# Kernel tuning notes

Measured on AMD Instinct MI355X. Metric: run time of the kernel, lower is better.

## Reference

```python
import jax, jax.numpy as jnp
import numpy as np

B, S = 128, 512          # batch, sequence length
VOCAB, E, H = 50000, 300, 64  # vocab, embed dim, hidden_size (num conv filters)
KMAX = H // 2 + 2 - 1    # largest kernel height = (H-1)//2 + 2 = 33


def setup_inputs() -> dict:
    key = jax.random.key(0)
    ks = jax.random.split(key, 6)
    x = jax.random.randint(ks[0], (B, 1, S), 0, VOCAB)                  # token ids, [B,1,S]
    emb = jax.random.normal(ks[1], (VOCAB, E), jnp.float32) * 0.1       # frozen embedding table
    Wconv = jax.random.normal(ks[2], (H, KMAX, E), jnp.float32) * 0.05  # padded conv kernels; conv i uses rows [:i//2+2]
    bconv = jax.random.normal(ks[3], (H,), jnp.float32) * 0.05
    Wlin = jax.random.normal(ks[4], (1, H), jnp.float32) * 0.1
    blin = jax.random.normal(ks[5], (1,), jnp.float32) * 0.1
    return {"x": x, "emb": emb, "Wconv": Wconv, "bconv": bconv, "Wlin": Wlin, "blin": blin}


def reference(x, emb, Wconv, bconv, Wlin, blin):
    # Embedding lookup: [B,1,S] -> [B,S,E] (channel dim of 1 is implicit)
    e = emb[x[:, 0]]
    feats = []
    for i in range(H):  # static loop over structurally distinct kernel sizes
        k = i // 2 + 2                      # kernel height for conv i
        w = Wconv[i, :k]                    # [k,E], valid (unpadded) kernel rows
        # Conv2d with kernel (k,E) on [B,1,S,E] == sliding dot product over positions.
        proj = jnp.einsum('bse,ke->bsk', e, w)          # [B,S,k]
        L = S - k + 1                                   # valid output length
        y = sum(proj[:, j:j + L, j] for j in range(k)) + bconv[i]  # [B,L]
        # tanh then topk(k=1, dim=1) == max over positions
        feats.append(jnp.max(jnp.tanh(y), axis=1))      # [B]
    h = jnp.stack(feats, axis=1)                        # [B,H]
    return jax.nn.sigmoid(h @ Wlin.T + blin)            # [B,1]
```

## Files before the change

### kernel.cpp

```cpp
#include <hip/hip_runtime.h>


#define SS     512
#define EE     300
#define HH     64
#define KMAXW  33
#define LP     168
#define HALFSZ 215040

typedef __attribute__((ext_vector_type(8))) short bf16x8;
typedef __attribute__((ext_vector_type(4))) float f32x4;

__device__ __forceinline__ unsigned short f2bf(float f) {
    unsigned u = __float_as_uint(f);
    unsigned r = ((u >> 16) & 1u) + 0x7FFFu;
    return (unsigned short)((u + r) >> 16);
}

__global__ __launch_bounds__(256) void prep_weights(const float* __restrict__ Wconv,
                                                    unsigned short* __restrict__ wsB) {
    int idx = blockIdx.x * 256 + threadIdx.x;
    int r    = idx & 7;
    int lane = (idx >> 3) & 63;
    int gs   = idx >> 9;
    int h    = gs / 420;
    int ww   = gs - h * 420;
    int g, t;
    if      (ww < 45)  { g = 0; t = ww;       }
    else if (ww < 130) { g = 1; t = ww - 45;  }
    else if (ww < 255) { g = 2; t = ww - 130; }
    else               { g = 3; t = ww - 255; }
    int j = t / 5, u = t - j * 5;
    int i  = g * 16 + (lane & 15);
    int ki = i / 2 + 2;
    int kk = (lane >> 4) * 8 + r;
    int e  = h * 160 + u * 32 + kk;
    float v = 0.f;
    if (e < EE && j < ki) v = Wconv[(i * KMAXW + j) * EE + e];
    wsB[idx] = f2bf(v);
}

#define MFMA(A, Bf, C) __builtin_amdgcn_mfma_f32_16x16x32_bf16((A), (Bf), (C), 0, 0, 0)

template<bool SEC>
__device__ __forceinline__ void do5(const unsigned short* lb, int j,
                                    const unsigned short* __restrict__ bp,
                                    int pbase, int sbase, f32x4 acc[3][2]) {
    #pragma unroll
    for (int u = 0; u < 5; ++u) {
        const unsigned short* lr = lb + j * LP + u * 32;
        bf16x8 a0 = *(const bf16x8*)(lr);
        bf16x8 a1 = *(const bf16x8*)(lr + 16 * LP);
        bf16x8 a2 = *(const bf16x8*)(lr + 32 * LP);
        bf16x8 bP = *(const bf16x8*)(bp + (pbase + j * 5 + u) * 512);
        acc[0][0] = MFMA(a0, bP, acc[0][0]);
        acc[1][0] = MFMA(a1, bP, acc[1][0]);
        acc[2][0] = MFMA(a2, bP, acc[2][0]);
        if (SEC) {
            bf16x8 bS = *(const bf16x8*)(bp + (sbase + j * 5 + u) * 512);
            acc[0][1] = MFMA(a0, bS, acc[0][1]);
            acc[1][1] = MFMA(a1, bS, acc[1][1]);
            acc[2][1] = MFMA(a2, bS, acc[2][1]);
        }
    }
}

__global__ __launch_bounds__(256, 3) void conv_fused(const int* __restrict__ x,
                                                     const float* __restrict__ emb,
                                                     const unsigned short* __restrict__ wsB,
                                                     const float* __restrict__ bconv,
                                                     float* __restrict__ wsF) {
    __shared__ __align__(16) unsigned short At[128 * LP];

    int b     = blockIdx.x / 6;
    int slice = blockIdx.x - b * 6;
    int t0    = slice * 96;

    int lane = threadIdx.x & 63;
    int w    = threadIdx.x >> 6;
    int p    = w >> 1;
    int h2   = w & 1;
    int m = lane & 15, q = lane >> 4;

    f32x4 acc[3][2] = {};

    const unsigned short* lb = At + (p * 48 + m) * LP + q * 8;

    for (int eh = 0; eh < 2; ++eh) {
        if (eh) __syncthreads();

        #pragma unroll
        for (int it = 0; it < 10; ++it) {
            int idx = threadIdx.x + it * 256;
            int rr = idx / 20, c = idx - rr * 20;
            int srow = t0 + rr;
            bf16x8 v = {0, 0, 0, 0, 0, 0, 0, 0};
            if (srow < SS) {
                int tok = x[b * SS + srow];
                const float* ep = emb + (long)tok * EE + eh * 160 + c * 8;
                if (eh == 0 || c < 17) {
                    float4 f0 = ((const float4*)ep)[0];
                    float4 f1 = ((const float4*)ep)[1];
                    v[0] = f2bf(f0.x); v[1] = f2bf(f0.y); v[2] = f2bf(f0.z); v[3] = f2bf(f0.w);
                    v[4] = f2bf(f1.x); v[5] = f2bf(f1.y); v[6] = f2bf(f1.z); v[7] = f2bf(f1.w);
                } else if (c == 17) {
                    float4 f0 = ((const float4*)ep)[0];
                    v[0] = f2bf(f0.x); v[1] = f2bf(f0.y); v[2] = f2bf(f0.z); v[3] = f2bf(f0.w);
                }
            }
            *(bf16x8*)&At[rr * LP + c * 8] = v;
        }
        __syncthreads();

        const unsigned short* bp = wsB + eh * HALFSZ + lane * 8;
        if (h2 == 0) {
            #pragma unroll 1
            for (int j = 0; j < 9;  ++j) do5<true >(lb, j, bp, 255, 0, acc);
            #pragma unroll 1
            for (int j = 9; j < 33; ++j) do5<false>(lb, j, bp, 255, 0, acc);
        } else {
            #pragma unroll 1
            for (int j = 0;  j < 17; ++j) do5<true >(lb, j, bp, 130, 45, acc);
            #pragma unroll 1
            for (int j = 17; j < 25; ++j) do5<false>(lb, j, bp, 130, 45, acc);
        }
    }

    int gid[2]; gid[0] = h2 ? 2 : 3; gid[1] = h2 ? 1 : 0;
    #pragma unroll
    for (int t = 0; t < 3; ++t) {
        int tb = t0 + p * 48 + t * 16 + q * 4;
        #pragma unroll
        for (int u2 = 0; u2 < 2; ++u2) {
            int i  = gid[u2] * 16 + m;
            int ki = i / 2 + 2;
            int tmax = SS - ki;
            float bc = bconv[i];
            float mx = -3.0e38f;
            #pragma unroll
            for (int r = 0; r < 4; ++r) {
                float v = tanhf(acc[t][u2][r] + bc);
                if (tb + r <= tmax) mx = fmaxf(mx, v);
            }
            mx = fmaxf(mx, __shfl_xor(mx, 16));
            mx = fmaxf(mx, __shfl_xor(mx, 32));
            if (q == 0) wsF[(b * HH + i) * 36 + slice * 6 + p * 3 + t] = mx;
        }
    }
}

__global__ __launch_bounds__(64) void final_linear(const float* __restrict__ wsF,
                                                   const float* __restrict__ Wlin,
                                                   const float* __restrict__ blin,
                                                   float* __restrict__ out) {
    int b = blockIdx.x;
    int i = threadIdx.x;
    const float* pp = wsF + (b * HH + i) * 36;
    float mx = pp[0];
    #pragma unroll
    for (int j = 1; j < 36; ++j) mx = fmaxf(mx, pp[j]);
    float v = mx * Wlin[i];
    #pragma unroll
    for (int off = 1; off < 64; off <<= 1) v += __shfl_xor(v, off);
    if (i == 0) out[b] = 1.0f / (1.0f + expf(-(v + blin[0])));
}

extern "C" void kernel_launch(void* const* d_in, const int* in_sizes, int n_in,
                              void* d_out, int out_size, void* d_ws, size_t ws_size,
                              hipStream_t stream) {
    const int*   x     = (const int*)d_in[0];
    const float* emb   = (const float*)d_in[1];
    const float* Wconv = (const float*)d_in[2];
    const float* bconv = (const float*)d_in[3];
    const float* Wlin  = (const float*)d_in[4];
    const float* blin  = (const float*)d_in[5];
    float* out = (float*)d_out;

    unsigned short* wsB = (unsigned short*)d_ws;
    float*          wsF = (float*)((char*)d_ws + (1u << 20));

    prep_weights<<<1680, 256, 0, stream>>>(Wconv, wsB);
    conv_fused<<<768, 256, 0, stream>>>(x, emb, wsB, bconv, wsF);
    final_linear<<<128, 64, 0, stream>>>(wsF, Wlin, blin, out);
}
```

Before: 195.1 us.

## Split conv work across waves by kernel-row range and reduce partials in LDS

Each wave used to own a fixed position slice and filter groups, which left the work unevenly split between waves. Now every wave covers all 96 positions and all filter groups but only a balanced subset of kernel-row offsets j. Partial sums are combined through LDS atomicAdd before the tanh and max epilogue. This balances MFMA work across the four waves and cuts the number of partial maxima written out, at the cost of a 6x4 accumulator array (more registers) and 96 float LDS atomics per lane.

Result: slower. 356.5 us (+82.8%).

```diff
diff --git a/kernel.cpp b/kernel.cpp
--- a/kernel.cpp
+++ b/kernel.cpp
@@ -7,6 +7,7 @@
 #define KMAXW  33
 #define LP     168
 #define HALFSZ 215040
+#define RP     68
 
 typedef __attribute__((ext_vector_type(8))) short bf16x8;
 typedef __attribute__((ext_vector_type(4))) float f32x4;
@@ -42,25 +43,29 @@
 
 #define MFMA(A, Bf, C) __builtin_amdgcn_mfma_f32_16x16x32_bf16((A), (Bf), (C), 0, 0, 0)
 
-template<bool SEC>
-__device__ __forceinline__ void do5(const unsigned short* lb, int j,
+template<int G0>
+__device__ __forceinline__ void seg(const unsigned short* __restrict__ ar0,
+                                    int jlo, int jhi,
                                     const unsigned short* __restrict__ bp,
-                                    int pbase, int sbase, f32x4 acc[3][2]) {
-    #pragma unroll
-    for (int u = 0; u < 5; ++u) {
-        const unsigned short* lr = lb + j * LP + u * 32;
-        bf16x8 a0 = *(const bf16x8*)(lr);
-        bf16x8 a1 = *(const bf16x8*)(lr + 16 * LP);
-        bf16x8 a2 = *(const bf16x8*)(lr + 32 * LP);
-        bf16x8 bP = *(const bf16x8*)(bp + (pbase + j * 5 + u) * 512);
-        acc[0][0] = MFMA(a0, bP, acc[0][0]);
-        acc[1][0] = MFMA(a1, bP, acc[1][0]);
-        acc[2][0] = MFMA(a2, bP, acc[2][0]);
-        if (SEC) {
-            bf16x8 bS = *(const bf16x8*)(bp + (sbase + j * 5 + u) * 512);
-            acc[0][1] = MFMA(a0, bS, acc[0][1]);
-            acc[1][1] = MFMA(a1, bS, acc[1][1]);
-            acc[2][1] = MFMA(a2, bS, acc[2][1]);
+                                    f32x4 acc[6][4]) {
+    #pragma unroll 1
+    for (int j = jlo; j < jhi; ++j) {
+        const unsigned short* ar = ar0 + j * LP;
+        const unsigned short* br = bp + j * 5 * 512;
+        #pragma unroll
+        for (int u = 0; u < 5; ++u) {
+            bf16x8 a[6];
+            #pragma unroll
+            for (int t = 0; t < 6; ++t)
+                a[t] = *(const bf16x8*)(ar + t * (16 * LP) + u * 32);
+            #pragma unroll
+            for (int g = G0; g < 4; ++g) {
+                constexpr int GBASE[4] = {0, 45, 130, 255};
+                bf16x8 bf = *(const bf16x8*)(br + (GBASE[g] + u) * 512);
+                #pragma unroll
+                for (int t = 0; t < 6; ++t)
+                    acc[t][g] = MFMA(a[t], bf, acc[t][g]);
+            }
         }
     }
 }
@@ -78,13 +83,11 @@
 
     int lane = threadIdx.x & 63;
     int w    = threadIdx.x >> 6;
-    int p    = w >> 1;
-    int h2   = w & 1;
     int m = lane & 15, q = lane >> 4;
 
-    f32x4 acc[3][2] = {};
-
-    const unsigned short* lb = At + (p * 48 + m) * LP + q * 8;
+    f32x4 acc[6][4] = {};
+
+    const unsigned short* ar0 = At + m * LP + q * 8;
 
     for (int eh = 0; eh < 2; ++eh) {
         if (eh) __syncthreads();
@@ -113,39 +116,57 @@
         __syncthreads();
 
         const unsigned short* bp = wsB + eh * HALFSZ + lane * 8;
-        if (h2 == 0) {
-            #pragma unroll 1
-            for (int j = 0; j < 9;  ++j) do5<true >(lb, j, bp, 255, 0, acc);
-            #pragma unroll 1
-            for (int j = 9; j < 33; ++j) do5<false>(lb, j, bp, 255, 0, acc);
+        if (w == 0) {
+            seg<0>(ar0, 0, 3,  bp, acc); seg<1>(ar0, 9, 12, bp, acc);
+        } else if (w == 1) {
+            seg<0>(ar0, 3, 6,  bp, acc); seg<1>(ar0, 12, 15, bp, acc);
+        } else if (w == 2) {
+            seg<0>(ar0, 6, 9,  bp, acc); seg<1>(ar0, 15, 17, bp, acc);
+            seg<3>(ar0, 25, 28, bp, acc);
         } else {
-            #pragma unroll 1
-            for (int j = 0;  j < 17; ++j) do5<true >(lb, j, bp, 130, 45, acc);
-            #pragma unroll 1
-            for (int j = 17; j < 25; ++j) do5<false>(lb, j, bp, 130, 45, acc);
+            seg<2>(ar0, 17, 25, bp, acc); seg<3>(ar0, 28, 33, bp, acc);
         }
     }
 
-    int gid[2]; gid[0] = h2 ? 2 : 3; gid[1] = h2 ? 1 : 0;
-    #pragma unroll
-    for (int t = 0; t < 3; ++t) {
-        int tb = t0 + p * 48 + t * 16 + q * 4;
+    __syncthreads();
+    float* red  = (float*)At;
+    float* red2 = red + 96 * RP;
+
+    #pragma unroll
+    for (int it = 0; it < 7; ++it) {
+        int idx = threadIdx.x + it * 256;
+        if (idx < 96 * RP / 4) ((float4*)red)[idx] = float4{0.f, 0.f, 0.f, 0.f};
+    }
+    __syncthreads();
+
+    #pragma unroll
+    for (int t = 0; t < 6; ++t)
         #pragma unroll
-        for (int u2 = 0; u2 < 2; ++u2) {
-            int i  = gid[u2] * 16 + m;
-            int ki = i / 2 + 2;
-            int tmax = SS - ki;
-            float bc = bconv[i];
-            float mx = -3.0e38f;
+        for (int g = 0; g < 4; ++g)
             #pragma unroll
-            for (int r = 0; r < 4; ++r) {
-                float v = tanhf(acc[t][u2][r] + bc);
-                if (tb + r <= tmax) mx = fmaxf(mx, v);
-            }
-            mx = fmaxf(mx, __shfl_xor(mx, 16));
-            mx = fmaxf(mx, __shfl_xor(mx, 32));
-            if (q == 0) wsF[(b * HH + i) * 36 + slice * 6 + p * 3 + t] = mx;
-        }
+            for (int r = 0; r < 4; ++r)
+                atomicAdd(&red[(t * 16 + q * 4 + r) * RP + g * 16 + m], acc[t][g][r]);
+    __syncthreads();
+
+    int f  = threadIdx.x & 63;
+    int rg = threadIdx.x >> 6;
+    int ki = (f >> 1) + 2;
+    int tmax = SS - ki;
+    float bc = bconv[f];
+    float mx = -3.0e38f;
+    #pragma unroll 1
+    for (int rr = 0; rr < 24; ++rr) {
+        int row = rg * 24 + rr;
+        int tb  = t0 + row;
+        float v = tanhf(red[row * RP + f] + bc);
+        if (tb <= tmax) mx = fmaxf(mx, v);
+    }
+    red2[rg * 64 + f] = mx;
+    __syncthreads();
+    if (threadIdx.x < 64) {
+        float v = fmaxf(fmaxf(red2[f], red2[64 + f]),
+                        fmaxf(red2[128 + f], red2[192 + f]));
+        wsF[(b * HH + f) * 6 + slice] = v;
     }
 }
 
@@ -155,10 +176,10 @@
                                                    float* __restrict__ out) {
     int b = blockIdx.x;
     int i = threadIdx.x;
-    const float* pp = wsF + (b * HH + i) * 36;
+    const float* pp = wsF + (b * HH + i) * 6;
     float mx = pp[0];
     #pragma unroll
-    for (int j = 1; j < 36; ++j) mx = fmaxf(mx, pp[j]);
+    for (int j = 1; j < 6; ++j) mx = fmaxf(mx, pp[j]);
     float v = mx * Wlin[i];
     #pragma unroll
     for (int off = 1; off < 64; off <<= 1) v += __shfl_xor(v, off);
```
